# Kernel optimization log

Hardware: AMD Instinct MI355X
Metric: run time of the kernel (lower is better)

## Reference

```python
import jax, jax.numpy as jnp
import numpy as np

NUM_EDGE_TYPES = 8
HIDDEN = 128
N_NODES = 50000
N_EDGES = 600000


def setup_inputs() -> dict:
    key = jax.random.key(0)
    ks = jax.random.split(key, 10)
    H = HIDDEN
    h = jax.random.normal(ks[0], (N_NODES, H), dtype=jnp.float32)
    edge_index = jax.random.randint(ks[1], (2, N_EDGES), 0, N_NODES, dtype=jnp.int32)
    edge_type = jax.random.randint(ks[2], (N_EDGES,), 0, NUM_EDGE_TYPES + 1, dtype=jnp.int32)
    s = 1.0 / np.sqrt(H)
    W_msg = jax.random.uniform(ks[3], (H, H), jnp.float32, -s, s)
    b_msg = jax.random.uniform(ks[4], (H,), jnp.float32, -s, s)
    edge_embed = jax.random.normal(ks[5], (NUM_EDGE_TYPES + 1, H), dtype=jnp.float32)
    W_ih = jax.random.uniform(ks[6], (3 * H, H), jnp.float32, -s, s)
    W_hh = jax.random.uniform(ks[7], (3 * H, H), jnp.float32, -s, s)
    b_ih = jax.random.uniform(ks[8], (3 * H,), jnp.float32, -s, s)
    b_hh = jax.random.uniform(ks[9], (3 * H,), jnp.float32, -s, s)
    return {"h": h, "edge_index": edge_index, "edge_type": edge_type,
            "num_nodes": N_NODES, "W_msg": W_msg, "b_msg": b_msg,
            "edge_embed": edge_embed, "W_ih": W_ih, "W_hh": W_hh,
            "b_ih": b_ih, "b_hh": b_hh}


def _gru_cell(x, h, W_ih, W_hh, b_ih, b_hh):
    # PyTorch GRUCell: gates ordered (r, z, n)
    H = h.shape[-1]
    gi = x @ W_ih.T + b_ih  # (N, 3H)
    gh = h @ W_hh.T + b_hh
    i_r, i_z, i_n = gi[:, :H], gi[:, H:2 * H], gi[:, 2 * H:]
    h_r, h_z, h_n = gh[:, :H], gh[:, H:2 * H], gh[:, 2 * H:]
    r = jax.nn.sigmoid(i_r + h_r)
    z = jax.nn.sigmoid(i_z + h_z)
    n = jnp.tanh(i_n + r * h_n)
    return (1.0 - z) * n + z * h


def reference(h, edge_index, edge_type, num_nodes, W_msg, b_msg, edge_embed, W_ih, W_hh, b_ih, b_hh):
    src = edge_index[0]
    dst = edge_index[1]
    # gather -> linear -> edge-type embed add
    src_h = h[src] @ W_msg.T + b_msg                      # (E, H)
    emb = edge_embed[jnp.clip(edge_type, 0, NUM_EDGE_TYPES)]  # (E, H)
    msg = src_h + emb
    # scatter-add into per-node message buffer
    messages = jax.ops.segment_sum(msg, dst, num_segments=num_nodes)  # (num_nodes, H)
    h_new = _gru_cell(messages, h[:num_nodes], W_ih, W_hh, b_ih, b_hh)
    result = jnp.zeros_like(h).at[:num_nodes].set(h_new)
    return result
```

## Files before the change

### kernel.cpp

```cpp
#include <hip/hip_runtime.h>
#include <math.h>

#define H 128
typedef unsigned int u32;
typedef unsigned long long u64;
typedef __attribute__((ext_vector_type(8))) short short8;
typedef __attribute__((ext_vector_type(4))) float floatx4;

#define XS_STRIDE 136
#define CS_STRIDE 40
#define ROWCAP 128

__device__ __forceinline__ float sigmoid_f(float x) {
    return 1.0f / (1.0f + __expf(-x));
}
__device__ __forceinline__ float tanh_f(float x) {
    float t = __expf(-2.0f * fabsf(x));
    float r = (1.0f - t) / (1.0f + t);
    return copysignf(r, x);
}
__device__ __forceinline__ unsigned short f2bf(float x) {
    u32 u = __float_as_uint(x);
    return (unsigned short)((u + 0x7fffu + ((u >> 16) & 1u)) >> 16);
}
__device__ __forceinline__ float bf2f(unsigned short s) {
    return __uint_as_float(((u32)s) << 16);
}
__device__ __forceinline__ float bf_lo32(u32 u) { return __uint_as_float(u << 16); }
__device__ __forceinline__ float bf_hi32(u32 u) { return __uint_as_float(u & 0xffff0000u); }

__global__ __launch_bounds__(256) void fused_pre_kernel(
    const float* __restrict__ h, unsigned short* __restrict__ h_b, int total8,
    int* __restrict__ head4, int* __restrict__ ohead, int N,
    const float* __restrict__ Wih, const float* __restrict__ Whh,
    const float* __restrict__ Wm,  const float* __restrict__ emb,
    const float* __restrict__ bm,
    unsigned short* __restrict__ Wcs, unsigned short* __restrict__ Whhs,
    unsigned short* __restrict__ embWs, int HB, int DB)
{
    int b = blockIdx.x;
    if (b < HB) {
        int idx = b * 256 + threadIdx.x;
        if (idx >= total8) return;
        const float4* p = (const float4*)(h + (size_t)idx * 8);
        float4 a = p[0], bb = p[1];
        short8 v;
        v[0] = (short)f2bf(a.x);  v[1] = (short)f2bf(a.y);
        v[2] = (short)f2bf(a.z);  v[3] = (short)f2bf(a.w);
        v[4] = (short)f2bf(bb.x); v[5] = (short)f2bf(bb.y);
        v[6] = (short)f2bf(bb.z); v[7] = (short)f2bf(bb.w);
        *(short8*)(h_b + (size_t)idx * 8) = v;
        return;
    }
    if (b < HB + DB) {
        int idx = (b - HB) * 256 + threadIdx.x;
        if (idx < 4 * N) head4[idx] = -1;
        else if (idx < 5 * N) ohead[idx - 4 * N] = -1;
        return;
    }
    int idx = (b - HB - DB) * 256 + threadIdx.x;
    if (idx < 49152) {
        int g = idx >> 7;
        int k = idx & 127;
        float acc = 0.f;
#pragma unroll 4
        for (int c = 0; c < H; ++c)
            acc += Wih[(size_t)g * H + c] * Wm[(size_t)c * H + k];
        int gate = g >> 7;
        int wi = g & 127;
        int j = wi >> 4, m = wi & 15;
        int kc = k >> 5, q = (k >> 3) & 3, i = k & 7;
        int l = q * 16 + m;
        Wcs[(size_t)(((gate * 8 + j) * 4 + kc) * 64 + l) * 8 + i] = f2bf(acc);
    } else if (idx < 61440) {
        int s = idx - 49152;
        int i = s & 7;
        int l = (s >> 3) & 63;
        int jb = s >> 9;
        int gate = jb >> 3, jj = jb & 7;
        int q = l >> 4, m = l & 15;
        int t = q * 8 + i;
        unsigned short v = 0;
        if (t < 9) {
            int g = gate * 128 + jj * 16 + m;
            float acc = 0.f;
#pragma unroll 4
            for (int jx = 0; jx < H; ++jx)
                acc += (emb[(size_t)t * H + jx] + bm[jx]) * Wih[(size_t)g * H + jx];
            v = f2bf(acc);
        }
        embWs[s] = v;
    } else if (idx < 67584) {
        int t2 = idx - 61440;
        int l  = t2 & 63;
        int kc = (t2 >> 6) & 3;
        int jr = t2 >> 8;
        int m = l & 15, q = l >> 4;
        size_t srco = (size_t)(jr * 16 + m) * H + kc * 32 + q * 8;
        const float4* s0 = (const float4*)(Whh + srco);
        float4 a = s0[0], bb = s0[1];
        short8 v;
        v[0] = (short)f2bf(a.x);  v[1] = (short)f2bf(a.y);
        v[2] = (short)f2bf(a.z);  v[3] = (short)f2bf(a.w);
        v[4] = (short)f2bf(bb.x); v[5] = (short)f2bf(bb.y);
        v[6] = (short)f2bf(bb.z); v[7] = (short)f2bf(bb.w);
        *(short8*)(Whhs + (size_t)t2 * 8) = v;
    }
}

__global__ __launch_bounds__(256) void fill_ll_kernel(
    const int* __restrict__ eidx, const int* __restrict__ etype,
    int* __restrict__ head4, int* __restrict__ nexte,
    int* __restrict__ packed, int E)
{
    int e = blockIdx.x * 256 + threadIdx.x;
    if (e >= E) return;
    int src = eidx[e];
    int dst = eidx[E + e];
    int t = etype[e];
    t = t < 0 ? 0 : (t > 8 ? 8 : t);
    packed[e] = src | (t << 24);
    int old = atomicExch(&head4[(size_t)dst * 4 + (e & 3)], e);
    nexte[e] = old;
}

__global__ __launch_bounds__(256) void ll2csr_kernel(
    const int* __restrict__ head4, int* __restrict__ nexte,
    const int* __restrict__ packed,
    int* __restrict__ slots, int* __restrict__ deg,
    int* __restrict__ ohead, int N)
{
    __shared__ int lbuf[256 * 33];

    int tid = threadIdx.x;
    int lane = tid & 63;
    int wv = tid >> 6;
    int n = (blockIdx.x * 4 + wv) * 16 + (lane >> 2);
    int cchain = lane & 3;
    bool valid = n < N;

    int e = valid ? head4[(size_t)n * 4 + cchain] : -1;
    int cnt = 0;
    int lbase = tid * 33;
    while (e >= 0) {
        int nx = nexte[e];
        int u = packed[e];
        if (cnt < 32) {
            lbuf[lbase + cnt] = u;
        } else {
            nexte[e] = atomicExch(&ohead[n], e);
        }
        cnt++;
        e = nx;
    }
    int cl = cnt < 32 ? cnt : 32;
    int base = lane & ~3;
    int c0 = __shfl(cl, base);
    int c1 = __shfl(cl, base + 1);
    int c2 = __shfl(cl, base + 2);
    int c3 = __shfl(cl, base + 3);
    int pc = (cchain > 0 ? c0 : 0) + (cchain > 1 ? c1 : 0) + (cchain > 2 ? c2 : 0);
    if (valid) {
        int* drow = slots + (size_t)n * ROWCAP + pc;
        for (int i = 0; i < cl; ++i) drow[i] = lbuf[lbase + i];
        if (cchain == 0) deg[n] = c0 + c1 + c2 + c3;
    }
}

__global__ __launch_bounds__(256) void gather_csr_kernel(
    const unsigned short* __restrict__ h_b,
    const int* __restrict__ deg, const int* __restrict__ slots,
    const int* __restrict__ ohead, const int* __restrict__ nexte,
    const int* __restrict__ packed,
    unsigned short* __restrict__ S_b, u64* __restrict__ cnt, int N)
{
    int n = blockIdx.x * 4 + (threadIdx.x >> 6);
    if (n >= N) return;
    int lane = threadIdx.x & 63;
    int m = deg[n];
    const int* row = slots + (size_t)n * ROWCAP;

    float ax = 0.f, ay = 0.f;
    u64 c = 0;
    int i = 0;
    for (; i + 8 <= m; i += 8) {
        int u0 = row[i + 0];
        int u1 = row[i + 1];
        int u2 = row[i + 2];
        int u3 = row[i + 3];
        int u4 = row[i + 4];
        int u5 = row[i + 5];
        int u6 = row[i + 6];
        int u7 = row[i + 7];
        u32 x0 = *((const u32*)(h_b + (size_t)(u0 & 0xffffff) * H) + lane);
        u32 x1 = *((const u32*)(h_b + (size_t)(u1 & 0xffffff) * H) + lane);
        u32 x2 = *((const u32*)(h_b + (size_t)(u2 & 0xffffff) * H) + lane);
        u32 x3 = *((const u32*)(h_b + (size_t)(u3 & 0xffffff) * H) + lane);
        u32 x4 = *((const u32*)(h_b + (size_t)(u4 & 0xffffff) * H) + lane);
        u32 x5 = *((const u32*)(h_b + (size_t)(u5 & 0xffffff) * H) + lane);
        u32 x6 = *((const u32*)(h_b + (size_t)(u6 & 0xffffff) * H) + lane);
        u32 x7 = *((const u32*)(h_b + (size_t)(u7 & 0xffffff) * H) + lane);
        c += (1ull << (7 * (u0 >> 24))) + (1ull << (7 * (u1 >> 24)))
           + (1ull << (7 * (u2 >> 24))) + (1ull << (7 * (u3 >> 24)))
           + (1ull << (7 * (u4 >> 24))) + (1ull << (7 * (u5 >> 24)))
           + (1ull << (7 * (u6 >> 24))) + (1ull << (7 * (u7 >> 24)));
        ax += bf_lo32(x0) + bf_lo32(x1) + bf_lo32(x2) + bf_lo32(x3)
            + bf_lo32(x4) + bf_lo32(x5) + bf_lo32(x6) + bf_lo32(x7);
        ay += bf_hi32(x0) + bf_hi32(x1) + bf_hi32(x2) + bf_hi32(x3)
            + bf_hi32(x4) + bf_hi32(x5) + bf_hi32(x6) + bf_hi32(x7);
    }
    for (; i + 4 <= m; i += 4) {
        int u0 = row[i + 0];
        int u1 = row[i + 1];
        int u2 = row[i + 2];
        int u3 = row[i + 3];
        u32 x0 = *((const u32*)(h_b + (size_t)(u0 & 0xffffff) * H) + lane);
        u32 x1 = *((const u32*)(h_b + (size_t)(u1 & 0xffffff) * H) + lane);
        u32 x2 = *((const u32*)(h_b + (size_t)(u2 & 0xffffff) * H) + lane);
        u32 x3 = *((const u32*)(h_b + (size_t)(u3 & 0xffffff) * H) + lane);
        c += (1ull << (7 * (u0 >> 24))) + (1ull << (7 * (u1 >> 24)))
           + (1ull << (7 * (u2 >> 24))) + (1ull << (7 * (u3 >> 24)));
        ax += bf_lo32(x0) + bf_lo32(x1) + bf_lo32(x2) + bf_lo32(x3);
        ay += bf_hi32(x0) + bf_hi32(x1) + bf_hi32(x2) + bf_hi32(x3);
    }
    for (; i < m; ++i) {
        int u = row[i];
        u32 x = *((const u32*)(h_b + (size_t)(u & 0xffffff) * H) + lane);
        c += 1ull << (7 * (u >> 24));
        ax += bf_lo32(x);
        ay += bf_hi32(x);
    }
    int oh = ohead[n];
    if (oh >= 0) {
        int ecur = oh;
        while (ecur >= 0) {
            int u = packed[ecur];
            u32 x = *((const u32*)(h_b + (size_t)(u & 0xffffff) * H) + lane);
            c += 1ull << (7 * (u >> 24));
            ax += bf_lo32(x);
            ay += bf_hi32(x);
            ecur = nexte[ecur];
        }
    }
    u32 o = (u32)f2bf(ax) | ((u32)f2bf(ay) << 16);
    *((u32*)(S_b + (size_t)n * H) + lane) = o;
    if (lane == 0) cnt[n] = c;
}

__global__ __launch_bounds__(256, 4) void gru_mfma_kernel(
    const unsigned short* __restrict__ S_b, const unsigned short* __restrict__ h_b,
    const unsigned short* __restrict__ Wcs, const unsigned short* __restrict__ Whhs,
    const unsigned short* __restrict__ embWs,
    const float* __restrict__ bih, const float* __restrict__ bhh,
    const u64* __restrict__ cnt,
    const int* __restrict__ numn, float* __restrict__ out, int N)
{
    __shared__ unsigned short xs[64 * XS_STRIDE];
    __shared__ unsigned short hsb[64 * XS_STRIDE];
    __shared__ unsigned short cs[64 * CS_STRIDE];

    int tid = threadIdx.x;
    int bx = blockIdx.x;
    int node0 = (bx >> 1) * 64;
    int jhalf = bx & 1;

    int lane = tid & 63;
    int wv = tid >> 6;
    int j = jhalf * 4 + wv;

    short8 er = *(const short8*)(embWs + (size_t)((0 * 8 + j) * 64 + lane) * 8);
    short8 ez = *(const short8*)(embWs + (size_t)((1 * 8 + j) * 64 + lane) * 8);
    short8 en = *(const short8*)(embWs + (size_t)((2 * 8 + j) * 64 + lane) * 8);

    for (int c = tid; c < 1024; c += 256) {
        int r = c >> 4;
        int k8 = (c & 15) << 3;
        int n = node0 + r;
        int nc = n < N ? n : N - 1;
        *(short8*)(&xs[r * XS_STRIDE + k8]) =
            *(const short8*)(S_b + (size_t)nc * H + k8);
        *(short8*)(&hsb[r * XS_STRIDE + k8]) =
            *(const short8*)(h_b + (size_t)nc * H + k8);
    }
    {
        int r = tid >> 2, tg = tid & 3;
        int n = node0 + r;
        u64 cv = cnt[n < N ? n : N - 1];
        short8 v = {0, 0, 0, 0, 0, 0, 0, 0};
        if (tg == 0) {
#pragma unroll
            for (int i = 0; i < 8; ++i)
                v[i] = (short)f2bf((float)((u32)(cv >> (7 * i)) & 127u));
        } else if (tg == 1) {
            v[0] = (short)f2bf((float)((u32)(cv >> 56) & 127u));
        }
        *(short8*)(&cs[r * CS_STRIDE + tg * 8]) = v;
    }
    __syncthreads();

    int am = lane & 15;
    int aq = lane >> 4;

    int num_nodes = numn[0];
    floatx4 zero = {0.f, 0.f, 0.f, 0.f};

    floatx4 aR[4], aZ[4], aIn[4], aHn[4];
#pragma unroll
    for (int rt = 0; rt < 4; ++rt) {
        short8 acn = *(const short8*)(&cs[(rt * 16 + am) * CS_STRIDE + aq * 8]);
        aR[rt]  = __builtin_amdgcn_mfma_f32_16x16x32_bf16(acn, er, zero, 0, 0, 0);
        aZ[rt]  = __builtin_amdgcn_mfma_f32_16x16x32_bf16(acn, ez, zero, 0, 0, 0);
        aIn[rt] = __builtin_amdgcn_mfma_f32_16x16x32_bf16(acn, en, zero, 0, 0, 0);
        aHn[rt] = zero;
    }
#pragma unroll
    for (int kc = 0; kc < 4; ++kc) {
        size_t c_r = (size_t)(((0 * 8 + j) * 4 + kc) * 64 + lane) * 8;
        size_t c_z = (size_t)(((1 * 8 + j) * 4 + kc) * 64 + lane) * 8;
        size_t c_n = (size_t)(((2 * 8 + j) * 4 + kc) * 64 + lane) * 8;
        short8 bir = *(const short8*)(Wcs + c_r);
        short8 bhr = *(const short8*)(Whhs + c_r);
        short8 biz = *(const short8*)(Wcs + c_z);
        short8 bhz = *(const short8*)(Whhs + c_z);
        short8 bin = *(const short8*)(Wcs + c_n);
        short8 bhn = *(const short8*)(Whhs + c_n);
#pragma unroll
        for (int rt = 0; rt < 4; ++rt) {
            int arow = rt * 16 + am;
            short8 axv = *(const short8*)(&xs[arow * XS_STRIDE + kc * 32 + aq * 8]);
            short8 ahv = *(const short8*)(&hsb[arow * XS_STRIDE + kc * 32 + aq * 8]);
            aR[rt]  = __builtin_amdgcn_mfma_f32_16x16x32_bf16(axv, bir, aR[rt], 0, 0, 0);
            aR[rt]  = __builtin_amdgcn_mfma_f32_16x16x32_bf16(ahv, bhr, aR[rt], 0, 0, 0);
            aZ[rt]  = __builtin_amdgcn_mfma_f32_16x16x32_bf16(axv, biz, aZ[rt], 0, 0, 0);
            aZ[rt]  = __builtin_amdgcn_mfma_f32_16x16x32_bf16(ahv, bhz, aZ[rt], 0, 0, 0);
            aIn[rt] = __builtin_amdgcn_mfma_f32_16x16x32_bf16(axv, bin, aIn[rt], 0, 0, 0);
            aHn[rt] = __builtin_amdgcn_mfma_f32_16x16x32_bf16(ahv, bhn, aHn[rt], 0, 0, 0);
        }
    }
    int c = j * 16 + am;
    float b_r = bih[c]       + bhh[c];
    float b_z = bih[128 + c] + bhh[128 + c];
    float b_in = bih[256 + c], b_hn = bhh[256 + c];
#pragma unroll
    for (int rt = 0; rt < 4; ++rt) {
#pragma unroll
        for (int q = 0; q < 4; ++q) {
            int m = rt * 16 + aq * 4 + q;
            int node = node0 + m;
            if (node < N) {
                float r  = sigmoid_f(aR[rt][q] + b_r);
                float z  = sigmoid_f(aZ[rt][q] + b_z);
                float nv = tanh_f((aIn[rt][q] + b_in) + r * (aHn[rt][q] + b_hn));
                float hv = bf2f(hsb[m * XS_STRIDE + c]);
                float o  = (1.0f - z) * nv + z * hv;
                out[(size_t)node * H + c] = (node < num_nodes) ? o : 0.0f;
            }
        }
    }
}

extern "C" void kernel_launch(void* const* d_in, const int* in_sizes, int n_in,
                              void* d_out, int out_size, void* d_ws, size_t ws_size,
                              hipStream_t stream) {
    const float* h    = (const float*)d_in[0];
    const int*  eidx  = (const int*)d_in[1];
    const int*  etype = (const int*)d_in[2];
    const int*  numn  = (const int*)d_in[3];
    const float* Wm   = (const float*)d_in[4];
    const float* bm   = (const float*)d_in[5];
    const float* emb  = (const float*)d_in[6];
    const float* Wih  = (const float*)d_in[7];
    const float* Whh  = (const float*)d_in[8];
    const float* bih  = (const float*)d_in[9];
    const float* bhh  = (const float*)d_in[10];

    int N = in_sizes[0] / H;
    int E = in_sizes[2];

    unsigned short* S_b   = (unsigned short*)d_ws;
    unsigned short* h_b   = S_b + (size_t)N * H;
    unsigned short* Wcs   = h_b + (size_t)N * H;
    unsigned short* Whhs  = Wcs + 3 * H * H;
    unsigned short* embWs = Whhs + 3 * H * H;
    u64* cnt    = (u64*)(embWs + 12288);
    int* deg    = (int*)(cnt + N);
    int* ohead  = deg + N;
    int* head4  = ohead + N;
    int* slots  = head4 + 4 * N;
    int* packed = slots + (size_t)N * ROWCAP;
    int* nexte  = packed + E;

    int total8 = N * H / 8;
    int HB = (total8 + 255) / 256;
    int DB = (5 * N + 255) / 256;
    int PB = 264;
    fused_pre_kernel<<<HB + DB + PB, 256, 0, stream>>>(
        h, h_b, total8, head4, ohead, N, Wih, Whh, Wm, emb, bm,
        Wcs, Whhs, embWs, HB, DB);

    fill_ll_kernel<<<(E + 255) / 256, 256, 0, stream>>>(
        eidx, etype, head4, nexte, packed, E);

    ll2csr_kernel<<<(N + 63) / 64, 256, 0, stream>>>(
        head4, nexte, packed, slots, deg, ohead, N);

    gather_csr_kernel<<<(N + 3) / 4, 256, 0, stream>>>(
        h_b, deg, slots, ohead, nexte, packed, S_b, cnt, N);

    int nblk = ((N + 63) / 64) * 2;
    gru_mfma_kernel<<<nblk, 256, 0, stream>>>(S_b, h_b, Wcs, Whhs, embWs,
                                              bih, bhh, cnt, numn, (float*)d_out, N);
}
```

Measured before the change: 206.3 us.

## Fuse linked-list-to-CSR conversion into gather kernel using shared-memory rows

Merges the ll2csr and gather kernels into one: each block walks the per-node edge linked lists for 64 nodes into a shared-memory row buffer, then its waves gather and sum the bf16 source rows. This removes the global slots/deg/ohead arrays, their initialisation, and one kernel launch with its global round trip. In exchange each block handles 64 nodes serially across 4 waves (16 nodes per wave), giving only about 782 blocks, and it uses shared-memory atomics, so there is less parallelism and gather latency hiding could suffer.

```diff
diff --git a/kernel.cpp b/kernel.cpp
--- a/kernel.cpp
+++ b/kernel.cpp
@@ -9,7 +9,7 @@
 
 #define XS_STRIDE 136
 #define CS_STRIDE 40
-#define ROWCAP 128
+#define ROWCAP 48
 
 __device__ __forceinline__ float sigmoid_f(float x) {
     return 1.0f / (1.0f + __expf(-x));
@@ -31,7 +31,7 @@
 
 __global__ __launch_bounds__(256) void fused_pre_kernel(
     const float* __restrict__ h, unsigned short* __restrict__ h_b, int total8,
-    int* __restrict__ head4, int* __restrict__ ohead, int N,
+    int* __restrict__ head4, int N,
     const float* __restrict__ Wih, const float* __restrict__ Whh,
     const float* __restrict__ Wm,  const float* __restrict__ emb,
     const float* __restrict__ bm,
@@ -55,7 +55,6 @@
     if (b < HB + DB) {
         int idx = (b - HB) * 256 + threadIdx.x;
         if (idx < 4 * N) head4[idx] = -1;
-        else if (idx < 5 * N) ohead[idx - 4 * N] = -1;
         return;
     }
     int idx = (b - HB - DB) * 256 + threadIdx.x;
@@ -124,127 +123,117 @@
     nexte[e] = old;
 }
 
-__global__ __launch_bounds__(256) void ll2csr_kernel(
+__global__ __launch_bounds__(256) void gather_fused_kernel(
+    const unsigned short* __restrict__ h_b,
     const int* __restrict__ head4, int* __restrict__ nexte,
-    const int* __restrict__ packed,
-    int* __restrict__ slots, int* __restrict__ deg,
-    int* __restrict__ ohead, int N)
-{
-    __shared__ int lbuf[256 * 33];
-
-    int tid = threadIdx.x;
-    int lane = tid & 63;
-    int wv = tid >> 6;
-    int n = (blockIdx.x * 4 + wv) * 16 + (lane >> 2);
-    int cchain = lane & 3;
-    bool valid = n < N;
-
-    int e = valid ? head4[(size_t)n * 4 + cchain] : -1;
-    int cnt = 0;
-    int lbase = tid * 33;
-    while (e >= 0) {
-        int nx = nexte[e];
-        int u = packed[e];
-        if (cnt < 32) {
-            lbuf[lbase + cnt] = u;
-        } else {
-            nexte[e] = atomicExch(&ohead[n], e);
-        }
-        cnt++;
-        e = nx;
-    }
-    int cl = cnt < 32 ? cnt : 32;
-    int base = lane & ~3;
-    int c0 = __shfl(cl, base);
-    int c1 = __shfl(cl, base + 1);
-    int c2 = __shfl(cl, base + 2);
-    int c3 = __shfl(cl, base + 3);
-    int pc = (cchain > 0 ? c0 : 0) + (cchain > 1 ? c1 : 0) + (cchain > 2 ? c2 : 0);
-    if (valid) {
-        int* drow = slots + (size_t)n * ROWCAP + pc;
-        for (int i = 0; i < cl; ++i) drow[i] = lbuf[lbase + i];
-        if (cchain == 0) deg[n] = c0 + c1 + c2 + c3;
-    }
-}
-
-__global__ __launch_bounds__(256) void gather_csr_kernel(
-    const unsigned short* __restrict__ h_b,
-    const int* __restrict__ deg, const int* __restrict__ slots,
-    const int* __restrict__ ohead, const int* __restrict__ nexte,
     const int* __restrict__ packed,
     unsigned short* __restrict__ S_b, u64* __restrict__ cnt, int N)
 {
-    int n = blockIdx.x * 4 + (threadIdx.x >> 6);
-    if (n >= N) return;
-    int lane = threadIdx.x & 63;
-    int m = deg[n];
-    const int* row = slots + (size_t)n * ROWCAP;
-
-    float ax = 0.f, ay = 0.f;
-    u64 c = 0;
-    int i = 0;
-    for (; i + 8 <= m; i += 8) {
-        int u0 = row[i + 0];
-        int u1 = row[i + 1];
-        int u2 = row[i + 2];
-        int u3 = row[i + 3];
-        int u4 = row[i + 4];
-        int u5 = row[i + 5];
-        int u6 = row[i + 6];
-        int u7 = row[i + 7];
-        u32 x0 = *((const u32*)(h_b + (size_t)(u0 & 0xffffff) * H) + lane);
-        u32 x1 = *((const u32*)(h_b + (size_t)(u1 & 0xffffff) * H) + lane);
-        u32 x2 = *((const u32*)(h_b + (size_t)(u2 & 0xffffff) * H) + lane);
-        u32 x3 = *((const u32*)(h_b + (size_t)(u3 & 0xffffff) * H) + lane);
-        u32 x4 = *((const u32*)(h_b + (size_t)(u4 & 0xffffff) * H) + lane);
-        u32 x5 = *((const u32*)(h_b + (size_t)(u5 & 0xffffff) * H) + lane);
-        u32 x6 = *((const u32*)(h_b + (size_t)(u6 & 0xffffff) * H) + lane);
-        u32 x7 = *((const u32*)(h_b + (size_t)(u7 & 0xffffff) * H) + lane);
-        c += (1ull << (7 * (u0 >> 24))) + (1ull << (7 * (u1 >> 24)))
-           + (1ull << (7 * (u2 >> 24))) + (1ull << (7 * (u3 >> 24)))
-           + (1ull << (7 * (u4 >> 24))) + (1ull << (7 * (u5 >> 24)))
-           + (1ull << (7 * (u6 >> 24))) + (1ull << (7 * (u7 >> 24)));
-        ax += bf_lo32(x0) + bf_lo32(x1) + bf_lo32(x2) + bf_lo32(x3)
-            + bf_lo32(x4) + bf_lo32(x5) + bf_lo32(x6) + bf_lo32(x7);
-        ay += bf_hi32(x0) + bf_hi32(x1) + bf_hi32(x2) + bf_hi32(x3)
-            + bf_hi32(x4) + bf_hi32(x5) + bf_hi32(x6) + bf_hi32(x7);
-    }
-    for (; i + 4 <= m; i += 4) {
-        int u0 = row[i + 0];
-        int u1 = row[i + 1];
-        int u2 = row[i + 2];
-        int u3 = row[i + 3];
-        u32 x0 = *((const u32*)(h_b + (size_t)(u0 & 0xffffff) * H) + lane);
-        u32 x1 = *((const u32*)(h_b + (size_t)(u1 & 0xffffff) * H) + lane);
-        u32 x2 = *((const u32*)(h_b + (size_t)(u2 & 0xffffff) * H) + lane);
-        u32 x3 = *((const u32*)(h_b + (size_t)(u3 & 0xffffff) * H) + lane);
-        c += (1ull << (7 * (u0 >> 24))) + (1ull << (7 * (u1 >> 24)))
-           + (1ull << (7 * (u2 >> 24))) + (1ull << (7 * (u3 >> 24)));
-        ax += bf_lo32(x0) + bf_lo32(x1) + bf_lo32(x2) + bf_lo32(x3);
-        ay += bf_hi32(x0) + bf_hi32(x1) + bf_hi32(x2) + bf_hi32(x3);
-    }
-    for (; i < m; ++i) {
-        int u = row[i];
-        u32 x = *((const u32*)(h_b + (size_t)(u & 0xffffff) * H) + lane);
-        c += 1ull << (7 * (u >> 24));
-        ax += bf_lo32(x);
-        ay += bf_hi32(x);
-    }
-    int oh = ohead[n];
-    if (oh >= 0) {
-        int ecur = oh;
-        while (ecur >= 0) {
-            int u = packed[ecur];
+    __shared__ int rowbuf[64 * ROWCAP];
+    __shared__ int lcnt[64];
+    __shared__ int lohead[64];
+
+    int tid = threadIdx.x;
+    if (tid < 64) { lcnt[tid] = 0; lohead[tid] = -1; }
+    __syncthreads();
+
+    {
+        int k = tid >> 2;
+        int cch = tid & 3;
+        int n = blockIdx.x * 64 + k;
+        if (n < N) {
+            int e = head4[(size_t)n * 4 + cch];
+            while (e >= 0) {
+                int nx = nexte[e];
+                int u = packed[e];
+                int p = atomicAdd(&lcnt[k], 1);
+                if (p < ROWCAP) {
+                    rowbuf[k * ROWCAP + p] = u;
+                } else {
+                    nexte[e] = atomicExch(&lohead[k], e);
+                }
+                e = nx;
+            }
+        }
+    }
+    __syncthreads();
+
+    int lane = tid & 63;
+    int wv = tid >> 6;
+    for (int t = 0; t < 16; ++t) {
+        int kk = wv * 16 + t;
+        int n = blockIdx.x * 64 + kk;
+        if (n >= N) break;
+        int m = lcnt[kk];
+        m = m < ROWCAP ? m : ROWCAP;
+        const int* row = &rowbuf[kk * ROWCAP];
+
+        float ax = 0.f, ay = 0.f;
+        u64 c = 0;
+        int i = 0;
+        for (; i + 8 <= m; i += 8) {
+            int u0 = row[i + 0];
+            int u1 = row[i + 1];
+            int u2 = row[i + 2];
+            int u3 = row[i + 3];
+            int u4 = row[i + 4];
+            int u5 = row[i + 5];
+            int u6 = row[i + 6];
+            int u7 = row[i + 7];
+            u32 x0 = *((const u32*)(h_b + (size_t)(u0 & 0xffffff) * H) + lane);
+            u32 x1 = *((const u32*)(h_b + (size_t)(u1 & 0xffffff) * H) + lane);
+            u32 x2 = *((const u32*)(h_b + (size_t)(u2 & 0xffffff) * H) + lane);
+            u32 x3 = *((const u32*)(h_b + (size_t)(u3 & 0xffffff) * H) + lane);
+            u32 x4 = *((const u32*)(h_b + (size_t)(u4 & 0xffffff) * H) + lane);
+            u32 x5 = *((const u32*)(h_b + (size_t)(u5 & 0xffffff) * H) + lane);
+            u32 x6 = *((const u32*)(h_b + (size_t)(u6 & 0xffffff) * H) + lane);
+            u32 x7 = *((const u32*)(h_b + (size_t)(u7 & 0xffffff) * H) + lane);
+            c += (1ull << (7 * (u0 >> 24))) + (1ull << (7 * (u1 >> 24)))
+               + (1ull << (7 * (u2 >> 24))) + (1ull << (7 * (u3 >> 24)))
+               + (1ull << (7 * (u4 >> 24))) + (1ull << (7 * (u5 >> 24)))
+               + (1ull << (7 * (u6 >> 24))) + (1ull << (7 * (u7 >> 24)));
+            ax += bf_lo32(x0) + bf_lo32(x1) + bf_lo32(x2) + bf_lo32(x3)
+                + bf_lo32(x4) + bf_lo32(x5) + bf_lo32(x6) + bf_lo32(x7);
+            ay += bf_hi32(x0) + bf_hi32(x1) + bf_hi32(x2) + bf_hi32(x3)
+                + bf_hi32(x4) + bf_hi32(x5) + bf_hi32(x6) + bf_hi32(x7);
+        }
+        for (; i + 4 <= m; i += 4) {
+            int u0 = row[i + 0];
+            int u1 = row[i + 1];
+            int u2 = row[i + 2];
+            int u3 = row[i + 3];
+            u32 x0 = *((const u32*)(h_b + (size_t)(u0 & 0xffffff) * H) + lane);
+            u32 x1 = *((const u32*)(h_b + (size_t)(u1 & 0xffffff) * H) + lane);
+            u32 x2 = *((const u32*)(h_b + (size_t)(u2 & 0xffffff) * H) + lane);
+            u32 x3 = *((const u32*)(h_b + (size_t)(u3 & 0xffffff) * H) + lane);
+            c += (1ull << (7 * (u0 >> 24))) + (1ull << (7 * (u1 >> 24)))
+               + (1ull << (7 * (u2 >> 24))) + (1ull << (7 * (u3 >> 24)));
+            ax += bf_lo32(x0) + bf_lo32(x1) + bf_lo32(x2) + bf_lo32(x3);
+            ay += bf_hi32(x0) + bf_hi32(x1) + bf_hi32(x2) + bf_hi32(x3);
+        }
+        for (; i < m; ++i) {
+            int u = row[i];
             u32 x = *((const u32*)(h_b + (size_t)(u & 0xffffff) * H) + lane);
             c += 1ull << (7 * (u >> 24));
             ax += bf_lo32(x);
             ay += bf_hi32(x);
-            ecur = nexte[ecur];
-        }
-    }
-    u32 o = (u32)f2bf(ax) | ((u32)f2bf(ay) << 16);
-    *((u32*)(S_b + (size_t)n * H) + lane) = o;
-    if (lane == 0) cnt[n] = c;
+        }
+        int oh = lohead[kk];
+        if (oh >= 0) {
+            int ecur = oh;
+            while (ecur >= 0) {
+                int u = packed[ecur];
+                u32 x = *((const u32*)(h_b + (size_t)(u & 0xffffff) * H) + lane);
+                c += 1ull << (7 * (u >> 24));
+                ax += bf_lo32(x);
+                ay += bf_hi32(x);
+                ecur = nexte[ecur];
+            }
+        }
+        u32 o = (u32)f2bf(ax) | ((u32)f2bf(ay) << 16);
+        *((u32*)(S_b + (size_t)n * H) + lane) = o;
+        if (lane == 0) cnt[n] = c;
+    }
 }
 
 __global__ __launch_bounds__(256, 4) void gru_mfma_kernel(
@@ -383,29 +372,23 @@
     unsigned short* Whhs  = Wcs + 3 * H * H;
     unsigned short* embWs = Whhs + 3 * H * H;
     u64* cnt    = (u64*)(embWs + 12288);
-    int* deg    = (int*)(cnt + N);
-    int* ohead  = deg + N;
-    int* head4  = ohead + N;
-    int* slots  = head4 + 4 * N;
-    int* packed = slots + (size_t)N * ROWCAP;
+    int* head4  = (int*)(cnt + N);
+    int* packed = head4 + 4 * N;
     int* nexte  = packed + E;
 
     int total8 = N * H / 8;
     int HB = (total8 + 255) / 256;
-    int DB = (5 * N + 255) / 256;
+    int DB = (4 * N + 255) / 256;
     int PB = 264;
     fused_pre_kernel<<<HB + DB + PB, 256, 0, stream>>>(
-        h, h_b, total8, head4, ohead, N, Wih, Whh, Wm, emb, bm,
+        h, h_b, total8, head4, N, Wih, Whh, Wm, emb, bm,
         Wcs, Whhs, embWs, HB, DB);
 
     fill_ll_kernel<<<(E + 255) / 256, 256, 0, stream>>>(
         eidx, etype, head4, nexte, packed, E);
 
-    ll2csr_kernel<<<(N + 63) / 64, 256, 0, stream>>>(
-        head4, nexte, packed, slots, deg, ohead, N);
-
-    gather_csr_kernel<<<(N + 3) / 4, 256, 0, stream>>>(
-        h_b, deg, slots, ohead, nexte, packed, S_b, cnt, N);
+    gather_fused_kernel<<<(N + 63) / 64, 256, 0, stream>>>(
+        h_b, head4, nexte, packed, S_b, cnt, N);
 
     int nblk = ((N + 63) / 64) * 2;
     gru_mfma_kernel<<<nblk, 256, 0, stream>>>(S_b, h_b, Wcs, Whhs, embWs,
```

Result: no change. 202.5 us (-1.8%).
